# Kernel tuning notes

Hardware: AMD Instinct MI355X
Metric: run time of the kernel (lower is better)

The kernel has to match this reference:

```python
import jax, jax.numpy as jnp
import numpy as np

# Static config (mirrors cfg.MODEL.LOSSES.Center.*)
ALPHA = 0.5
BETA = 0.1
MARGIN = 50.0
SCALE = 1.0
HARD_MINING = False
B, D, C = 512, 512, 100000


def setup_inputs() -> dict:
    key = jax.random.key(0)
    k1, k2, k3 = jax.random.split(key, 3)
    features = jax.random.normal(k1, (B, D), dtype=jnp.float32)
    labels = jax.random.randint(k2, (B,), 0, C, dtype=jnp.int32)
    centers = jax.random.normal(k3, (C, D), dtype=jnp.float32)
    return {"features": features, "labels": labels, "centers": centers}


def softmax_weights(dist, mask):
    # dist: (B, B) (negative distances), mask: (B, B) in {0, 1}
    min_v = jnp.min(dist * mask, axis=1, keepdims=True)
    numerator = jnp.exp(dist - min_v) * mask  # mask also zeroes out masked entries
    Z = jnp.sum(numerator, axis=1, keepdims=True) + 1e-6
    return numerator / Z


def reference(features, labels, centers):
    labels = labels.astype(jnp.int32)
    # gather, detached (torch: self.centers[labels].detach())
    cg = jax.lax.stop_gradient(centers[labels])  # (B, D)
    delta1 = cg - features  # (B, D)

    center_diff = cg[:, None, :] - cg[None, :, :]  # (B, B, D)
    mask = (labels[None, :] != labels[:, None]).astype(jnp.float32)  # (B, B)
    center_dist = jnp.sqrt(jnp.sum(jnp.square(center_diff), axis=2))  # (B, B)
    mask = mask * (center_dist <= MARGIN).astype(jnp.float32)

    W = softmax_weights(-center_dist, mask)  # (B, B)
    delta2 = jnp.sum(center_diff * W[:, :, None], axis=1)  # (B, D)
    # torch: if mask.sum() < 1: delta2 = zeros
    delta2 = jnp.where(jnp.sum(mask) < 1.0, jnp.zeros_like(delta2), delta2)

    new_vals = cg - ALPHA * delta1 - BETA * delta2  # (B, D)
    new_centers = centers.at[labels].set(jax.lax.stop_gradient(new_vals))

    dist = jnp.clip(jnp.square(cg - features), 1e-12, 1e12)
    loss = jnp.mean(dist) * SCALE
    return loss, new_centers
```

## Files before the change

kernel.cpp:

```cpp
#include <hip/hip_runtime.h>

#define B 512
#define D 512
#define NC 100000
#define BETA 0.1f
#define MARGIN 50.0f
#define TPB 256
#define N4 (NC * D / 4)
#define C0 4266666
#define C1 8533332

typedef float f4 __attribute__((ext_vector_type(4)));

__device__ __forceinline__ void copy_chunk(const f4* __restrict__ src, float* __restrict__ dst,
                                           int lo, int hi, int widx, int wstride)
{
    int i = lo + widx;
    for (; i + 7 * wstride < hi; i += 8 * wstride) {
        f4 v[8];
        #pragma unroll
        for (int u = 0; u < 8; ++u) v[u] = __builtin_nontemporal_load(&src[i + u * wstride]);
        #pragma unroll
        for (int u = 0; u < 8; ++u) {
            float* d = dst + 4 * (size_t)(i + u * wstride);
            __builtin_nontemporal_store(v[u].x, d + 0);
            __builtin_nontemporal_store(v[u].y, d + 1);
            __builtin_nontemporal_store(v[u].z, d + 2);
            __builtin_nontemporal_store(v[u].w, d + 3);
        }
    }
    for (; i < hi; i += wstride) {
        f4 v = __builtin_nontemporal_load(&src[i]);
        float* d = dst + 4 * (size_t)i;
        __builtin_nontemporal_store(v.x, d + 0);
        __builtin_nontemporal_store(v.y, d + 1);
        __builtin_nontemporal_store(v.z, d + 2);
        __builtin_nontemporal_store(v.w, d + 3);
    }
}

__global__ __launch_bounds__(TPB) void k0_gather(
    const float* __restrict__ centers, const float* __restrict__ features,
    const int* __restrict__ labels, float* __restrict__ cgbuf,
    float* __restrict__ rowLoss, int* __restrict__ winner, float* __restrict__ outC)
{
    const int b = blockIdx.x, t = threadIdx.x;
    if (b < B) {
        __shared__ float red[TPB];
        __shared__ int labs[B];
        __shared__ int wsh;
        labs[t] = labels[t]; labs[t + 256] = labels[t + 256];
        if (t == 0) wsh = 1;
        __syncthreads();
        const int i = b;
        const int li = labs[i];
        const float2* crow = (const float2*)(centers + (size_t)li * D);
        const float2* frow = (const float2*)(features + (size_t)i * D);
        float2 c = crow[t], f = frow[t];
        ((float2*)(cgbuf + (size_t)i * D))[t] = c;
        float dx = c.x - f.x, dy = c.y - f.y;
        red[t] = fminf(fmaxf(dx * dx, 1e-12f), 1e12f) + fminf(fmaxf(dy * dy, 1e-12f), 1e12f);
        for (int j = i + 1 + t; j < B; j += TPB)
            if (labs[j] == li) wsh = 0;
        __syncthreads();
        for (int s = 128; s; s >>= 1) { if (t < s) red[t] += red[t + s]; __syncthreads(); }
        if (t == 0) { rowLoss[i] = red[0]; winner[i] = wsh; }
    } else {
        copy_chunk((const f4*)centers, outC, 0, C0, (b - 512) * TPB + t, 1536 * TPB);
    }
}

__global__ __launch_bounds__(TPB) void k1_pairdist(
    const float* __restrict__ centers, const float* __restrict__ cgbuf,
    float* __restrict__ dist, float* __restrict__ outC)
{
    const int b = blockIdx.x, t = threadIdx.x;
    if (b < 256) {
        __shared__ float As[16][33];
        __shared__ float Bs[16][33];
        const int bi = b >> 4, bj = b & 15;
        const int tx = t & 15, ty = t >> 4;
        float a00 = 0.f, a01 = 0.f, a10 = 0.f, a11 = 0.f;
        for (int k0 = 0; k0 < D; k0 += 16) {
            #pragma unroll
            for (int it = 0; it < 2; ++it) {
                int idx = t + it * 256;
                int r = idx >> 4, kk = idx & 15;
                As[kk][r] = cgbuf[(size_t)(bi * 32 + r) * D + k0 + kk];
                Bs[kk][r] = cgbuf[(size_t)(bj * 32 + r) * D + k0 + kk];
            }
            __syncthreads();
            #pragma unroll
            for (int kk = 0; kk < 16; ++kk) {
                float x0 = As[kk][ty * 2], x1 = As[kk][ty * 2 + 1];
                float y0 = Bs[kk][tx * 2], y1 = Bs[kk][tx * 2 + 1];
                float d00 = x0 - y0, d01 = x0 - y1, d10 = x1 - y0, d11 = x1 - y1;
                a00 += d00 * d00; a01 += d01 * d01; a10 += d10 * d10; a11 += d11 * d11;
            }
            __syncthreads();
        }
        int r0 = bi * 32 + ty * 2, c0 = bj * 32 + tx * 2;
        dist[r0 * B + c0]           = sqrtf(a00);
        dist[r0 * B + c0 + 1]       = sqrtf(a01);
        dist[(r0 + 1) * B + c0]     = sqrtf(a10);
        dist[(r0 + 1) * B + c0 + 1] = sqrtf(a11);
    } else {
        copy_chunk((const f4*)centers, outC, C0, C1, (b - 256) * TPB + t, 1792 * TPB);
    }
}

__global__ __launch_bounds__(TPB) void k2_softmax(
    const float* __restrict__ centers, const float* __restrict__ dist,
    const int* __restrict__ labels, float* __restrict__ Wm,
    float* __restrict__ rowS, float* __restrict__ rowCnt, float* __restrict__ outC)
{
    const int b = blockIdx.x, t = threadIdx.x;
    if (b < B) {
        __shared__ float red[TPB];
        __shared__ int labs[B];
        labs[t] = labels[t]; labs[t + 256] = labels[t + 256];
        __syncthreads();
        const int i = b;
        const int li = labs[i];
        float d0 = dist[i * B + t], d1 = dist[i * B + t + 256];
        int m0 = (labs[t] != li) && (d0 <= MARGIN);
        int m1 = (labs[t + 256] != li) && (d1 <= MARGIN);
        red[t] = fmaxf(m0 ? d0 : 0.f, m1 ? d1 : 0.f); __syncthreads();
        for (int s = 128; s; s >>= 1) { if (t < s) red[t] = fmaxf(red[t], red[t + s]); __syncthreads(); }
        float maxd = red[0]; __syncthreads();
        float n0 = m0 ? expf(maxd - d0) : 0.f;
        float n1 = m1 ? expf(maxd - d1) : 0.f;
        red[t] = n0 + n1; __syncthreads();
        for (int s = 128; s; s >>= 1) { if (t < s) red[t] += red[t + s]; __syncthreads(); }
        float Z = red[0] + 1e-6f; __syncthreads();
        float invZ = 1.f / Z;
        Wm[i * B + t]       = n0 * invZ;
        Wm[i * B + t + 256] = n1 * invZ;
        red[t] = (float)(m0 + m1); __syncthreads();
        for (int s = 128; s; s >>= 1) { if (t < s) red[t] += red[t + s]; __syncthreads(); }
        if (t == 0) { rowS[i] = (Z - 1e-6f) * invZ; rowCnt[i] = red[0]; }
    } else {
        copy_chunk((const f4*)centers, outC, C1, N4, (b - 512) * TPB + t, 1536 * TPB);
    }
}

__global__ __launch_bounds__(TPB) void k3_final(
    const float* __restrict__ features, const int* __restrict__ labels,
    const float* __restrict__ cgbuf, const float* __restrict__ Wm,
    const float* __restrict__ rowS, const float* __restrict__ rowCnt,
    const int* __restrict__ winner, const float* __restrict__ rowLoss,
    float* __restrict__ out, float* __restrict__ outC)
{
    const int b = blockIdx.x, t = threadIdx.x;
    __shared__ float red[TPB];
    if (b < 256) {
        __shared__ float As[16][33];
        __shared__ float Bs[16][33];
        __shared__ float fsh;
        red[t] = rowCnt[t] + rowCnt[t + 256]; __syncthreads();
        for (int s = 128; s; s >>= 1) { if (t < s) red[t] += red[t + s]; __syncthreads(); }
        if (t == 0) fsh = (red[0] < 1.0f) ? 0.f : 1.f;
        __syncthreads();
        const float flagv = fsh;
        const int bi = b >> 4, bj = b & 15;
        const int tx = t & 15, ty = t >> 4;
        float a00 = 0.f, a01 = 0.f, a10 = 0.f, a11 = 0.f;
        for (int j0 = 0; j0 < B; j0 += 16) {
            #pragma unroll
            for (int it = 0; it < 2; ++it) {
                int idx = t + it * 256;
                int r = idx >> 4, jj = idx & 15;
                As[jj][r] = Wm[(size_t)(bi * 32 + r) * B + j0 + jj];
                int c = idx & 31, jj2 = idx >> 5;
                Bs[jj2][c] = cgbuf[(size_t)(j0 + jj2) * D + bj * 32 + c];
            }
            __syncthreads();
            #pragma unroll
            for (int kk = 0; kk < 16; ++kk) {
                float w0 = As[kk][ty * 2], w1 = As[kk][ty * 2 + 1];
                float c0 = Bs[kk][tx * 2], c1 = Bs[kk][tx * 2 + 1];
                a00 += w0 * c0; a01 += w0 * c1; a10 += w1 * c0; a11 += w1 * c1;
            }
            __syncthreads();
        }
        const int i0 = bi * 32 + ty * 2, i1 = i0 + 1;
        const int dcol = bj * 32 + tx * 2;
        float s0 = rowS[i0], s1 = rowS[i1];
        int wn0 = winner[i0], wn1 = winner[i1];
        size_t orow0 = (size_t)labels[i0] * D, orow1 = (size_t)labels[i1] * D;
        float c, f;
        c = cgbuf[(size_t)i0 * D + dcol];     f = features[(size_t)i0 * D + dcol];
        float val00 = 0.5f * (c + f) - BETA * flagv * (s0 * c - a00);
        c = cgbuf[(size_t)i0 * D + dcol + 1]; f = features[(size_t)i0 * D + dcol + 1];
        float val01 = 0.5f * (c + f) - BETA * flagv * (s0 * c - a01);
        c = cgbuf[(size_t)i1 * D + dcol];     f = features[(size_t)i1 * D + dcol];
        float val10 = 0.5f * (c + f) - BETA * flagv * (s1 * c - a10);
        c = cgbuf[(size_t)i1 * D + dcol + 1]; f = features[(size_t)i1 * D + dcol + 1];
        float val11 = 0.5f * (c + f) - BETA * flagv * (s1 * c - a11);
        if (wn0) { outC[orow0 + dcol] = val00; outC[orow0 + dcol + 1] = val01; }
        if (wn1) { outC[orow1 + dcol] = val10; outC[orow1 + dcol + 1] = val11; }
    } else {
        red[t] = rowLoss[t] + rowLoss[t + 256]; __syncthreads();
        for (int s = 128; s; s >>= 1) { if (t < s) red[t] += red[t + s]; __syncthreads(); }
        if (t == 0) out[0] = red[0] * (1.0f / ((float)B * (float)D));
    }
}

extern "C" void kernel_launch(void* const* d_in, const int* in_sizes, int n_in,
                              void* d_out, int out_size, void* d_ws, size_t ws_size,
                              hipStream_t stream)
{
    const float* features = (const float*)d_in[0];
    const int*   labels   = (const int*)d_in[1];
    const float* centers  = (const float*)d_in[2];

    float* out  = (float*)d_out;
    float* outC = out + 1;

    char* ws = (char*)d_ws;
    float* cgbuf   = (float*)(ws);
    float* dist    = (float*)(ws + 1048576);
    float* Wm      = (float*)(ws + 2097152);
    float* rowLoss = (float*)(ws + 3145728);
    float* rowS    = (float*)(ws + 3147776);
    float* rowCnt  = (float*)(ws + 3149824);
    int*   winner  = (int*)  (ws + 3151872);

    k0_gather<<<2048, TPB, 0, stream>>>(centers, features, labels, cgbuf, rowLoss, winner, outC);
    k1_pairdist<<<2048, TPB, 0, stream>>>(centers, cgbuf, dist, outC);
    k2_softmax<<<2048, TPB, 0, stream>>>(centers, dist, labels, Wm, rowS, rowCnt, outC);
    k3_final<<<257, TPB, 0, stream>>>(features, labels, cgbuf, Wm, rowS, rowCnt,
                                      winner, rowLoss, out, outC);
}
```

Measured before the change: 125.3 us.

## Align centers copy to output by shifting three floats, spread it over four kernels

The output centers array starts at out+1, so stores were misaligned and split into four scalar nontemporal stores. The copy now shifts by three floats so each destination f4 is 16-byte aligned, with unaligned memcpy loads from the source. The boundary elements are copied separately. The copy is also split across four kernels, including the GEMM kernel. The scatter of updated rows moves to a new fifth kernel that runs after the bulk copy, which adds a launch and a staging buffer for the updated values.

```diff
diff --git a/kernel.cpp b/kernel.cpp
--- a/kernel.cpp
+++ b/kernel.cpp
@@ -6,36 +6,31 @@
 #define BETA 0.1f
 #define MARGIN 50.0f
 #define TPB 256
-#define N4 (NC * D / 4)
-#define C0 4266666
-#define C1 8533332
+#define NFLOAT (NC * D)
+#define N4V 12799999
+#define K0E 2954290
+#define K1E 6400962
+#define K2E 9355252
 
 typedef float f4 __attribute__((ext_vector_type(4)));
 
-__device__ __forceinline__ void copy_chunk(const f4* __restrict__ src, float* __restrict__ dst,
-                                           int lo, int hi, int widx, int wstride)
-{
+__device__ __forceinline__ void copy_shifted(const float* __restrict__ srcF, float* __restrict__ dstF,
+                                             int lo, int hi, int widx, int wstride)
+{
+    const float* s = srcF + 3;
+    f4* d = (f4*)(dstF + 3);
     int i = lo + widx;
     for (; i + 7 * wstride < hi; i += 8 * wstride) {
         f4 v[8];
         #pragma unroll
-        for (int u = 0; u < 8; ++u) v[u] = __builtin_nontemporal_load(&src[i + u * wstride]);
+        for (int u = 0; u < 8; ++u) __builtin_memcpy(&v[u], s + 4 * (size_t)(i + u * wstride), 16);
         #pragma unroll
-        for (int u = 0; u < 8; ++u) {
-            float* d = dst + 4 * (size_t)(i + u * wstride);
-            __builtin_nontemporal_store(v[u].x, d + 0);
-            __builtin_nontemporal_store(v[u].y, d + 1);
-            __builtin_nontemporal_store(v[u].z, d + 2);
-            __builtin_nontemporal_store(v[u].w, d + 3);
-        }
+        for (int u = 0; u < 8; ++u) __builtin_nontemporal_store(v[u], d + (i + u * wstride));
     }
     for (; i < hi; i += wstride) {
-        f4 v = __builtin_nontemporal_load(&src[i]);
-        float* d = dst + 4 * (size_t)i;
-        __builtin_nontemporal_store(v.x, d + 0);
-        __builtin_nontemporal_store(v.y, d + 1);
-        __builtin_nontemporal_store(v.z, d + 2);
-        __builtin_nontemporal_store(v.w, d + 3);
+        f4 v;
+        __builtin_memcpy(&v, s + 4 * (size_t)i, 16);
+        __builtin_nontemporal_store(v, d + i);
     }
 }
 
@@ -66,7 +61,7 @@
         for (int s = 128; s; s >>= 1) { if (t < s) red[t] += red[t + s]; __syncthreads(); }
         if (t == 0) { rowLoss[i] = red[0]; winner[i] = wsh; }
     } else {
-        copy_chunk((const f4*)centers, outC, 0, C0, (b - 512) * TPB + t, 1536 * TPB);
+        copy_shifted(centers, outC, 0, K0E, (b - 512) * TPB + t, 1536 * TPB);
     }
 }
 
@@ -105,7 +100,7 @@
         dist[(r0 + 1) * B + c0]     = sqrtf(a10);
         dist[(r0 + 1) * B + c0 + 1] = sqrtf(a11);
     } else {
-        copy_chunk((const f4*)centers, outC, C0, C1, (b - 256) * TPB + t, 1792 * TPB);
+        copy_shifted(centers, outC, K0E, K1E, (b - 256) * TPB + t, 1792 * TPB);
     }
 }
 
@@ -140,20 +135,20 @@
         for (int s = 128; s; s >>= 1) { if (t < s) red[t] += red[t + s]; __syncthreads(); }
         if (t == 0) { rowS[i] = (Z - 1e-6f) * invZ; rowCnt[i] = red[0]; }
     } else {
-        copy_chunk((const f4*)centers, outC, C1, N4, (b - 512) * TPB + t, 1536 * TPB);
-    }
-}
-
-__global__ __launch_bounds__(TPB) void k3_final(
-    const float* __restrict__ features, const int* __restrict__ labels,
+        copy_shifted(centers, outC, K1E, K2E, (b - 512) * TPB + t, 1536 * TPB);
+    }
+}
+
+__global__ __launch_bounds__(TPB) void k3_gemm(
+    const float* __restrict__ features, const float* __restrict__ centers,
     const float* __restrict__ cgbuf, const float* __restrict__ Wm,
     const float* __restrict__ rowS, const float* __restrict__ rowCnt,
-    const int* __restrict__ winner, const float* __restrict__ rowLoss,
+    const float* __restrict__ rowLoss, float* __restrict__ vals,
     float* __restrict__ out, float* __restrict__ outC)
 {
     const int b = blockIdx.x, t = threadIdx.x;
-    __shared__ float red[TPB];
     if (b < 256) {
+        __shared__ float red[TPB];
         __shared__ float As[16][33];
         __shared__ float Bs[16][33];
         __shared__ float fsh;
@@ -186,24 +181,39 @@
         const int i0 = bi * 32 + ty * 2, i1 = i0 + 1;
         const int dcol = bj * 32 + tx * 2;
         float s0 = rowS[i0], s1 = rowS[i1];
-        int wn0 = winner[i0], wn1 = winner[i1];
-        size_t orow0 = (size_t)labels[i0] * D, orow1 = (size_t)labels[i1] * D;
         float c, f;
         c = cgbuf[(size_t)i0 * D + dcol];     f = features[(size_t)i0 * D + dcol];
-        float val00 = 0.5f * (c + f) - BETA * flagv * (s0 * c - a00);
+        vals[(size_t)i0 * D + dcol]     = 0.5f * (c + f) - BETA * flagv * (s0 * c - a00);
         c = cgbuf[(size_t)i0 * D + dcol + 1]; f = features[(size_t)i0 * D + dcol + 1];
-        float val01 = 0.5f * (c + f) - BETA * flagv * (s0 * c - a01);
+        vals[(size_t)i0 * D + dcol + 1] = 0.5f * (c + f) - BETA * flagv * (s0 * c - a01);
         c = cgbuf[(size_t)i1 * D + dcol];     f = features[(size_t)i1 * D + dcol];
-        float val10 = 0.5f * (c + f) - BETA * flagv * (s1 * c - a10);
+        vals[(size_t)i1 * D + dcol]     = 0.5f * (c + f) - BETA * flagv * (s1 * c - a10);
         c = cgbuf[(size_t)i1 * D + dcol + 1]; f = features[(size_t)i1 * D + dcol + 1];
-        float val11 = 0.5f * (c + f) - BETA * flagv * (s1 * c - a11);
-        if (wn0) { outC[orow0 + dcol] = val00; outC[orow0 + dcol + 1] = val01; }
-        if (wn1) { outC[orow1 + dcol] = val10; outC[orow1 + dcol + 1] = val11; }
-    } else {
+        vals[(size_t)i1 * D + dcol + 1] = 0.5f * (c + f) - BETA * flagv * (s1 * c - a11);
+    } else if (b == 256) {
+        __shared__ float red[TPB];
         red[t] = rowLoss[t] + rowLoss[t + 256]; __syncthreads();
         for (int s = 128; s; s >>= 1) { if (t < s) red[t] += red[t + s]; __syncthreads(); }
         if (t == 0) out[0] = red[0] * (1.0f / ((float)B * (float)D));
-    }
+        if (t == 1) { outC[0] = centers[0]; outC[1] = centers[1]; outC[2] = centers[2]; }
+        if (t == 2) { outC[NFLOAT - 1] = centers[NFLOAT - 1]; }
+    } else {
+        copy_shifted(centers, outC, K2E, N4V, (b - 257) * TPB + t, 1791 * TPB);
+    }
+}
+
+__global__ __launch_bounds__(TPB) void k4_scatter(
+    const float* __restrict__ vals, const int* __restrict__ labels,
+    const int* __restrict__ winner, float* __restrict__ outC)
+{
+    const int b = blockIdx.x, t = threadIdx.x;
+    const int i = b * 2 + (t >> 7);
+    const int dcol = (t & 127) * 4;
+    if (!winner[i]) return;
+    f4 v;
+    __builtin_memcpy(&v, &vals[(size_t)i * D + dcol], 16);
+    float* dst = outC + (size_t)labels[i] * D + dcol;
+    __builtin_memcpy(dst, &v, 16);
 }
 
 extern "C" void kernel_launch(void* const* d_in, const int* in_sizes, int n_in,
@@ -221,14 +231,16 @@
     float* cgbuf   = (float*)(ws);
     float* dist    = (float*)(ws + 1048576);
     float* Wm      = (float*)(ws + 2097152);
-    float* rowLoss = (float*)(ws + 3145728);
-    float* rowS    = (float*)(ws + 3147776);
-    float* rowCnt  = (float*)(ws + 3149824);
-    int*   winner  = (int*)  (ws + 3151872);
+    float* vals    = (float*)(ws + 3145728);
+    float* rowLoss = (float*)(ws + 4194304);
+    float* rowS    = (float*)(ws + 4196352);
+    float* rowCnt  = (float*)(ws + 4198400);
+    int*   winner  = (int*)  (ws + 4200448);
 
     k0_gather<<<2048, TPB, 0, stream>>>(centers, features, labels, cgbuf, rowLoss, winner, outC);
     k1_pairdist<<<2048, TPB, 0, stream>>>(centers, cgbuf, dist, outC);
     k2_softmax<<<2048, TPB, 0, stream>>>(centers, dist, labels, Wm, rowS, rowCnt, outC);
-    k3_final<<<257, TPB, 0, stream>>>(features, labels, cgbuf, Wm, rowS, rowCnt,
-                                      winner, rowLoss, out, outC);
-}
+    k3_gemm<<<2048, TPB, 0, stream>>>(features, centers, cgbuf, Wm, rowS, rowCnt,
+                                      rowLoss, vals, out, outC);
+    k4_scatter<<<256, TPB, 0, stream>>>(vals, labels, winner, outC);
+}
```

Result: faster. 102.5 us (-18.2%).
